# Optimization experiments

Hardware: AMD Instinct MI355X
Metric: run time of the kernel (lower is better)

The kernel has to match this reference:

```python
import jax, jax.numpy as jnp
import numpy as np

ATTN_SIZE = 64
ENC_SIZE = 512
HIDDEN_SIZE = 512
L, B = 2048, 64


def setup_inputs() -> dict:
    key = jax.random.key(0)
    k1, k2, k3, k4, k5, k6 = jax.random.split(key, 6)
    enc_outputs = jax.random.normal(k1, (L, B, ENC_SIZE), dtype=jnp.float32)
    lens = jax.random.randint(k2, (B,), 1, L + 1, dtype=jnp.int32)
    hidden_states = jax.random.normal(k3, (B, HIDDEN_SIZE), dtype=jnp.float32)
    # Xavier-normal params as in reset_params()
    W_enc = jax.random.normal(k4, (ENC_SIZE, ATTN_SIZE), dtype=jnp.float32) * np.sqrt(2.0 / (ENC_SIZE + ATTN_SIZE))
    W_hidden = jax.random.normal(k5, (HIDDEN_SIZE, ATTN_SIZE), dtype=jnp.float32) * np.sqrt(2.0 / (HIDDEN_SIZE + ATTN_SIZE))
    b_attn = jnp.zeros((ATTN_SIZE,), dtype=jnp.float32)
    v = jax.random.normal(k6, (ATTN_SIZE,), dtype=jnp.float32)
    return {"enc_outputs": enc_outputs, "lens": lens, "hidden_states": hidden_states,
            "W_enc": W_enc, "b_attn": b_attn, "W_hidden": W_hidden, "v": v}


def reference(enc_outputs, lens, hidden_states, W_enc, b_attn, W_hidden, v):
    l = enc_outputs.shape[0]
    # parts: (l, b, attn_size) — projection of encoder outputs
    parts = jnp.einsum('lbd,da->lba', enc_outputs, W_enc) + b_attn
    # additive (Bahdanau) score: tanh(parts + h @ W_hidden) . v -> (l, b)
    hid = hidden_states @ W_hidden  # (b, attn_size)
    scores = jnp.sum(jnp.tanh(parts + hid[None, :, :]) * v, axis=2)
    # faithful mask: 1.0 at valid positions, -inf at padding (original adds 1, a
    # constant shift that softmax cancels, but we reproduce the exact math)
    valid = jnp.arange(l, dtype=lens.dtype)[:, None] < lens[None, :]  # (l, b)
    mask = jnp.where(valid, jnp.float32(1.0), -jnp.inf)
    w = jax.nn.softmax(scores + mask, axis=0)  # softmax over sequence dim
    # weighted sum over sequence: (b, d)
    return jnp.einsum('lb,lbd->bd', w, enc_outputs)
```

## Files before the change

kernel.cpp:

```cpp
#include <hip/hip_runtime.h>
#include <hip/hip_bf16.h>
#include <math.h>

#define L_DIM 2048
#define B_DIM 64
#define D_DIM 512
#define A_DIM 64

#define SUB_L 16
#define CHUNK_L 64
#define N_SUB (CHUNK_L / SUB_L)
#define N_CHUNK (L_DIM / CHUNK_L)
#define EPAD 520

typedef __attribute__((ext_vector_type(8))) short bf16x8;
typedef __attribute__((ext_vector_type(4))) float f32x4;

__device__ __forceinline__ void split_bf16(float x, short& hi, short& lo) {
    __hip_bfloat16 h = __float2bfloat16(x);
    float hf = __bfloat162float(h);
    __hip_bfloat16 l = __float2bfloat16(x - hf);
    hi = *reinterpret_cast<short*>(&h);
    lo = *reinterpret_cast<short*>(&l);
}

__device__ __forceinline__ void split4(const float4& x, short4& h, short4& l) {
    split_bf16(x.x, h.x, l.x);
    split_bf16(x.y, h.y, l.y);
    split_bf16(x.z, h.z, l.z);
    split_bf16(x.w, h.w, l.w);
}

__global__ void hb_kernel(const float* __restrict__ hidden,
                          const float* __restrict__ Wh,
                          const float* __restrict__ battn,
                          float* __restrict__ hb) {
    const int b = blockIdx.x;
    const int a = threadIdx.x;
    const float* hrow = hidden + b * D_DIM;
    float acc = battn[a];
#pragma unroll 8
    for (int d = 0; d < D_DIM; ++d) acc += hrow[d] * Wh[d * A_DIM + a];
    hb[b * A_DIM + a] = acc;
}

__global__ __launch_bounds__(256) void wt_kernel(const float* __restrict__ We,
                                                 short* __restrict__ wt_hi,
                                                 short* __restrict__ wt_lo) {
    const int idx = blockIdx.x * 256 + threadIdx.x;
    const int a = idx & 63;
    const int d = idx >> 6;
    float x = We[d * A_DIM + a];
    short h, l;
    split_bf16(x, h, l);
    wt_hi[a * D_DIM + d] = h;
    wt_lo[a * D_DIM + d] = l;
}

__global__ __launch_bounds__(256) void fused_kernel(
    const float* __restrict__ enc, const short* __restrict__ wt_hi,
    const short* __restrict__ wt_lo, const float* __restrict__ hb,
    const float* __restrict__ v, const int* __restrict__ lens,
    float* __restrict__ Om, float* __restrict__ mz) {
    const int c = blockIdx.x;
    const int b = blockIdx.y;
    const int tid = threadIdx.x;
    const int wave = tid >> 6;
    const int lane = tid & 63;
    const int quad = lane >> 4;
    const int l15 = lane & 15;
    const int po = tid & 127;
    const int par = tid >> 7;

    __shared__ short Ehi[SUB_L][EPAD];
    __shared__ short Elo[SUB_L][EPAD];
    __shared__ float sred[SUB_L][4];
    __shared__ float wl[SUB_L];
    __shared__ float msc[2];
    __shared__ float ored[D_DIM];

    const int len_b = lens[b];
    const int a_col = wave * 16 + l15;
    const float hb0 = hb[b * A_DIM + a_col];
    const float v0 = v[a_col];

    float4 Oacc = {0.f, 0.f, 0.f, 0.f};
    float mA = -INFINITY, ZA = 0.f;

    const float* encb = enc + (size_t)c * CHUNK_L * B_DIM * D_DIM +
                        (size_t)b * D_DIM + po * 4;
    const size_t ROWSTRIDE = (size_t)B_DIM * D_DIM;

    float4 cur[8], nxt[8];
#pragma unroll
    for (int j = 0; j < 8; ++j)
        cur[j] = *(const float4*)(encb + (size_t)(2 * j + par) * ROWSTRIDE);

    const short* bh = wt_hi + (size_t)a_col * D_DIM + quad * 8;
    const short* bl = wt_lo + (size_t)a_col * D_DIM + quad * 8;

#pragma unroll 1
    for (int sub = 0; sub < N_SUB; ++sub) {
#pragma unroll
        for (int j = 0; j < 8; ++j) {
            const int li = 2 * j + par;
            short4 h4, l4;
            split4(cur[j], h4, l4);
            *(short4*)&Ehi[li][po * 4] = h4;
            *(short4*)&Elo[li][po * 4] = l4;
        }
        __syncthreads();

        if (sub + 1 < N_SUB) {
            const float* p = encb + (size_t)(sub + 1) * SUB_L * ROWSTRIDE;
#pragma unroll
            for (int j = 0; j < 8; ++j)
                nxt[j] = *(const float4*)(p + (size_t)(2 * j + par) * ROWSTRIDE);
        }

        f32x4 acc = {0.f, 0.f, 0.f, 0.f};
#pragma unroll 4
        for (int s = 0; s < 16; ++s) {
            const int k = s * 32;
            const bf16x8 Ah = *(const bf16x8*)&Ehi[l15][k + quad * 8];
            const bf16x8 Al = *(const bf16x8*)&Elo[l15][k + quad * 8];
            const bf16x8 Bh = *(const bf16x8*)(bh + k);
            const bf16x8 Bl = *(const bf16x8*)(bl + k);
            acc = __builtin_amdgcn_mfma_f32_16x16x32_bf16(Ah, Bh, acc, 0, 0, 0);
            acc = __builtin_amdgcn_mfma_f32_16x16x32_bf16(Ah, Bl, acc, 0, 0, 0);
            acc = __builtin_amdgcn_mfma_f32_16x16x32_bf16(Al, Bh, acc, 0, 0, 0);
        }

#pragma unroll
        for (int r = 0; r < 4; ++r) {
            float t = tanhf(acc[r] + hb0) * v0;
            t += __shfl_xor(t, 1);
            t += __shfl_xor(t, 2);
            t += __shfl_xor(t, 4);
            t += __shfl_xor(t, 8);
            if (l15 == 0) sred[quad * 4 + r][wave] = t;
        }
        __syncthreads();

        if (tid < SUB_L) {
            const int lg = c * CHUNK_L + sub * SUB_L + tid;
            float s = sred[tid][0] + sred[tid][1] + sred[tid][2] + sred[tid][3];
            s = (lg < len_b) ? (s + 1.0f) : -INFINITY;
            float m = s;
            m = fmaxf(m, __shfl_xor(m, 1));
            m = fmaxf(m, __shfl_xor(m, 2));
            m = fmaxf(m, __shfl_xor(m, 4));
            m = fmaxf(m, __shfl_xor(m, 8));
            const float w = (m == -INFINITY) ? 0.f : expf(s - m);
            wl[tid] = w;
            float z = w;
            z += __shfl_xor(z, 1);
            z += __shfl_xor(z, 2);
            z += __shfl_xor(z, 4);
            z += __shfl_xor(z, 8);
            if (tid == 0) { msc[0] = m; msc[1] = z; }
        }
        __syncthreads();

        const float m_sub = msc[0], Z_sub = msc[1];
        const float mN = fmaxf(mA, m_sub);
        const float cA = (mA == -INFINITY) ? 0.f : expf(mA - mN);
        const float cS = (m_sub == -INFINITY) ? 0.f : expf(m_sub - mN);
        Oacc.x *= cA; Oacc.y *= cA; Oacc.z *= cA; Oacc.w *= cA;
#pragma unroll
        for (int j = 0; j < 8; ++j) {
            const float w = cS * wl[2 * j + par];
            Oacc.x += w * cur[j].x;
            Oacc.y += w * cur[j].y;
            Oacc.z += w * cur[j].z;
            Oacc.w += w * cur[j].w;
        }
        ZA = cA * ZA + cS * Z_sub;
        mA = mN;

#pragma unroll
        for (int j = 0; j < 8; ++j) cur[j] = nxt[j];
    }

    if (par == 0) *(float4*)&ored[po * 4] = Oacc;
    __syncthreads();
    if (par == 1) {
        const float4 o0 = *(const float4*)&ored[po * 4];
        float4 r;
        r.x = o0.x + Oacc.x;
        r.y = o0.y + Oacc.y;
        r.z = o0.z + Oacc.z;
        r.w = o0.w + Oacc.w;
        *(float4*)(Om + ((size_t)b * N_CHUNK + c) * D_DIM + po * 4) = r;
    }
    if (tid == 0) {
        mz[((size_t)b * N_CHUNK + c) * 2 + 0] = mA;
        mz[((size_t)b * N_CHUNK + c) * 2 + 1] = ZA;
    }
}

__global__ __launch_bounds__(256) void combine_kernel(
    const float* __restrict__ Om, const float* __restrict__ mz,
    float* __restrict__ out) {
    const int b = blockIdx.x;
    const int tid = threadIdx.x;
    __shared__ float coef[N_CHUNK];
    __shared__ float sinv;

    if (tid < 32) {
        const float m = mz[((size_t)b * N_CHUNK + tid) * 2 + 0];
        const float Z = mz[((size_t)b * N_CHUNK + tid) * 2 + 1];
        float mm = m;
        mm = fmaxf(mm, __shfl_xor(mm, 1));
        mm = fmaxf(mm, __shfl_xor(mm, 2));
        mm = fmaxf(mm, __shfl_xor(mm, 4));
        mm = fmaxf(mm, __shfl_xor(mm, 8));
        mm = fmaxf(mm, __shfl_xor(mm, 16));
        const float cc = (m == -INFINITY) ? 0.f : expf(m - mm);
        coef[tid] = cc;
        float s = cc * Z;
        s += __shfl_xor(s, 1);
        s += __shfl_xor(s, 2);
        s += __shfl_xor(s, 4);
        s += __shfl_xor(s, 8);
        s += __shfl_xor(s, 16);
        if (tid == 0) sinv = 1.0f / s;
    }
    __syncthreads();

    const float* base = Om + (size_t)b * N_CHUNK * D_DIM + tid * 2;
    float ox = 0.f, oy = 0.f;
#pragma unroll 8
    for (int cc = 0; cc < N_CHUNK; ++cc) {
        const float2 x = *(const float2*)(base + cc * D_DIM);
        ox += coef[cc] * x.x;
        oy += coef[cc] * x.y;
    }
    const float s = sinv;
    *(float2*)(out + (size_t)b * D_DIM + tid * 2) = make_float2(ox * s, oy * s);
}

extern "C" void kernel_launch(void* const* d_in, const int* in_sizes, int n_in,
                              void* d_out, int out_size, void* d_ws, size_t ws_size,
                              hipStream_t stream) {
    const float* enc    = (const float*)d_in[0];
    const int*   lens   = (const int*)d_in[1];
    const float* hidden = (const float*)d_in[2];
    const float* We     = (const float*)d_in[3];
    const float* battn  = (const float*)d_in[4];
    const float* Wh     = (const float*)d_in[5];
    const float* v      = (const float*)d_in[6];
    float* out = (float*)d_out;

    char* w8 = (char*)d_ws;
    float* hb    = (float*)(w8 + 0);
    short* wt_hi = (short*)(w8 + 16 * 1024);
    short* wt_lo = (short*)(w8 + 80 * 1024);
    float* mz    = (float*)(w8 + 144 * 1024);
    float* Om    = (float*)(w8 + 160 * 1024);

    hb_kernel<<<B_DIM, A_DIM, 0, stream>>>(hidden, Wh, battn, hb);
    wt_kernel<<<(D_DIM * A_DIM) / 256, 256, 0, stream>>>(We, wt_hi, wt_lo);
    fused_kernel<<<dim3(N_CHUNK, B_DIM), 256, 0, stream>>>(
        enc, wt_hi, wt_lo, hb, v, lens, Om, mz);
    combine_kernel<<<B_DIM, 256, 0, stream>>>(Om, mz, out);
}
```

Measured before the change: 498.0 us.

## Hoist B fragments to registers, double-buffer LDS, split MFMA accumulators

```diff
diff --git a/kernel.cpp b/kernel.cpp
--- a/kernel.cpp
+++ b/kernel.cpp
@@ -29,6 +29,17 @@
     split_bf16(x.y, h.y, l.y);
     split_bf16(x.z, h.z, l.z);
     split_bf16(x.w, h.w, l.w);
+}
+
+__device__ __forceinline__ float bf_hi_lo(short h, short l) {
+    unsigned uh = ((unsigned)(unsigned short)h) << 16;
+    unsigned ul = ((unsigned)(unsigned short)l) << 16;
+    return __uint_as_float(uh) + __uint_as_float(ul);
+}
+
+__device__ __forceinline__ void lds_barrier() {
+    asm volatile("s_waitcnt lgkmcnt(0)" ::: "memory");
+    __builtin_amdgcn_s_barrier();
 }
 
 __global__ void hb_kernel(const float* __restrict__ hidden,
@@ -57,7 +68,7 @@
     wt_lo[a * D_DIM + d] = l;
 }
 
-__global__ __launch_bounds__(256) void fused_kernel(
+__global__ __launch_bounds__(256, 2) void fused_kernel(
     const float* __restrict__ enc, const short* __restrict__ wt_hi,
     const short* __restrict__ wt_lo, const float* __restrict__ hb,
     const float* __restrict__ v, const int* __restrict__ lens,
@@ -72,8 +83,8 @@
     const int po = tid & 127;
     const int par = tid >> 7;
 
-    __shared__ short Ehi[SUB_L][EPAD];
-    __shared__ short Elo[SUB_L][EPAD];
+    __shared__ short Ehi[2][SUB_L][EPAD];
+    __shared__ short Elo[2][SUB_L][EPAD];
     __shared__ float sred[SUB_L][4];
     __shared__ float wl[SUB_L];
     __shared__ float msc[2];
@@ -84,6 +95,15 @@
     const float hb0 = hb[b * A_DIM + a_col];
     const float v0 = v[a_col];
 
+    const short* bh = wt_hi + (size_t)a_col * D_DIM + quad * 8;
+    const short* bl = wt_lo + (size_t)a_col * D_DIM + quad * 8;
+    bf16x8 Bh[16], Bl[16];
+#pragma unroll
+    for (int s = 0; s < 16; ++s) {
+        Bh[s] = *(const bf16x8*)(bh + s * 32);
+        Bl[s] = *(const bf16x8*)(bl + s * 32);
+    }
+
     float4 Oacc = {0.f, 0.f, 0.f, 0.f};
     float mA = -INFINITY, ZA = 0.f;
 
@@ -91,56 +111,55 @@
                         (size_t)b * D_DIM + po * 4;
     const size_t ROWSTRIDE = (size_t)B_DIM * D_DIM;
 
-    float4 cur[8], nxt[8];
+    float4 buf[8];
 #pragma unroll
     for (int j = 0; j < 8; ++j)
-        cur[j] = *(const float4*)(encb + (size_t)(2 * j + par) * ROWSTRIDE);
-
-    const short* bh = wt_hi + (size_t)a_col * D_DIM + quad * 8;
-    const short* bl = wt_lo + (size_t)a_col * D_DIM + quad * 8;
-
-#pragma unroll 1
+        buf[j] = *(const float4*)(encb + (size_t)(2 * j + par) * ROWSTRIDE);
+
+#pragma unroll 2
     for (int sub = 0; sub < N_SUB; ++sub) {
+        const int cb = sub & 1;
+
 #pragma unroll
         for (int j = 0; j < 8; ++j) {
             const int li = 2 * j + par;
             short4 h4, l4;
-            split4(cur[j], h4, l4);
-            *(short4*)&Ehi[li][po * 4] = h4;
-            *(short4*)&Elo[li][po * 4] = l4;
-        }
-        __syncthreads();
+            split4(buf[j], h4, l4);
+            *(short4*)&Ehi[cb][li][po * 4] = h4;
+            *(short4*)&Elo[cb][li][po * 4] = l4;
+        }
+        lds_barrier();
 
         if (sub + 1 < N_SUB) {
             const float* p = encb + (size_t)(sub + 1) * SUB_L * ROWSTRIDE;
 #pragma unroll
             for (int j = 0; j < 8; ++j)
-                nxt[j] = *(const float4*)(p + (size_t)(2 * j + par) * ROWSTRIDE);
-        }
-
-        f32x4 acc = {0.f, 0.f, 0.f, 0.f};
-#pragma unroll 4
+                buf[j] = *(const float4*)(p + (size_t)(2 * j + par) * ROWSTRIDE);
+        }
+
+        f32x4 a0 = {0.f, 0.f, 0.f, 0.f};
+        f32x4 a1 = {0.f, 0.f, 0.f, 0.f};
+        f32x4 a2 = {0.f, 0.f, 0.f, 0.f};
+#pragma unroll
         for (int s = 0; s < 16; ++s) {
             const int k = s * 32;
-            const bf16x8 Ah = *(const bf16x8*)&Ehi[l15][k + quad * 8];
-            const bf16x8 Al = *(const bf16x8*)&Elo[l15][k + quad * 8];
-            const bf16x8 Bh = *(const bf16x8*)(bh + k);
-            const bf16x8 Bl = *(const bf16x8*)(bl + k);
-            acc = __builtin_amdgcn_mfma_f32_16x16x32_bf16(Ah, Bh, acc, 0, 0, 0);
-            acc = __builtin_amdgcn_mfma_f32_16x16x32_bf16(Ah, Bl, acc, 0, 0, 0);
-            acc = __builtin_amdgcn_mfma_f32_16x16x32_bf16(Al, Bh, acc, 0, 0, 0);
+            const bf16x8 Ah = *(const bf16x8*)&Ehi[cb][l15][k + quad * 8];
+            const bf16x8 Al = *(const bf16x8*)&Elo[cb][l15][k + quad * 8];
+            a0 = __builtin_amdgcn_mfma_f32_16x16x32_bf16(Ah, Bh[s], a0, 0, 0, 0);
+            a1 = __builtin_amdgcn_mfma_f32_16x16x32_bf16(Ah, Bl[s], a1, 0, 0, 0);
+            a2 = __builtin_amdgcn_mfma_f32_16x16x32_bf16(Al, Bh[s], a2, 0, 0, 0);
         }
 
 #pragma unroll
         for (int r = 0; r < 4; ++r) {
-            float t = tanhf(acc[r] + hb0) * v0;
+            float t = tanhf(a0[r] + a1[r] + a2[r] + hb0) * v0;
             t += __shfl_xor(t, 1);
             t += __shfl_xor(t, 2);
             t += __shfl_xor(t, 4);
             t += __shfl_xor(t, 8);
             if (l15 == 0) sred[quad * 4 + r][wave] = t;
         }
-        __syncthreads();
+        lds_barrier();
 
         if (tid < SUB_L) {
             const int lg = c * CHUNK_L + sub * SUB_L + tid;
@@ -160,7 +179,7 @@
             z += __shfl_xor(z, 8);
             if (tid == 0) { msc[0] = m; msc[1] = z; }
         }
-        __syncthreads();
+        lds_barrier();
 
         const float m_sub = msc[0], Z_sub = msc[1];
         const float mN = fmaxf(mA, m_sub);
@@ -169,17 +188,17 @@
         Oacc.x *= cA; Oacc.y *= cA; Oacc.z *= cA; Oacc.w *= cA;
 #pragma unroll
         for (int j = 0; j < 8; ++j) {
-            const float w = cS * wl[2 * j + par];
-            Oacc.x += w * cur[j].x;
-            Oacc.y += w * cur[j].y;
-            Oacc.z += w * cur[j].z;
-            Oacc.w += w * cur[j].w;
+            const int li = 2 * j + par;
+            const float w = cS * wl[li];
+            const short4 h4 = *(const short4*)&Ehi[cb][li][po * 4];
+            const short4 l4 = *(const short4*)&Elo[cb][li][po * 4];
+            Oacc.x += w * bf_hi_lo(h4.x, l4.x);
+            Oacc.y += w * bf_hi_lo(h4.y, l4.y);
+            Oacc.z += w * bf_hi_lo(h4.z, l4.z);
+            Oacc.w += w * bf_hi_lo(h4.w, l4.w);
         }
         ZA = cA * ZA + cS * Z_sub;
         mA = mN;
-
-#pragma unroll
-        for (int j = 0; j < 8; ++j) cur[j] = nxt[j];
     }
 
     if (par == 0) *(float4*)&ored[po * 4] = Oacc;
```

Result: faster. 436.3 us (-12.4%).
